# Kernel optimization log

Hardware: AMD Instinct MI355X
Metric: run time of the kernel (lower is better)

The kernel has to match this reference:

```python
import jax, jax.numpy as jnp
import numpy as np

B, S, D = 4, 2048, 1024
H, DK, DV = 16, 64, 64


def setup_inputs() -> dict:
    key = jax.random.key(0)
    ks = jax.random.split(key, 7)
    scale = 0.02
    emb = jax.random.normal(ks[0], (B, S, D), dtype=jnp.float32)
    # per-head projection weights stacked over heads: [H, D, DK/DV]
    Wq = jax.random.normal(ks[1], (H, D, DK), dtype=jnp.float32) * scale
    Wk = jax.random.normal(ks[2], (H, D, DK), dtype=jnp.float32) * scale
    Wv = jax.random.normal(ks[3], (H, D, DV), dtype=jnp.float32) * scale
    # output projection (nn.Linear(d_model, d_model)): weight [D, D] (input-major) + bias
    Wo = jax.random.normal(ks[4], (D, D), dtype=jnp.float32) * scale
    bo = jax.random.normal(ks[5], (D,), dtype=jnp.float32) * scale
    return {"emb": emb, "Wq": Wq, "Wk": Wk, "Wv": Wv, "Wo": Wo, "bo": bo}


def reference(emb, Wq, Wk, Wv, Wo, bo):
    # Per-head projections, batched over heads: [B,H,S,dk]
    q = jnp.einsum("bsd,hdk->bhsk", emb, Wq)
    k = jnp.einsum("bsd,hdk->bhsk", emb, Wk)
    v = jnp.einsum("bsd,hdv->bhsv", emb, Wv)
    # Scaled dot-product with causal mask (bool_mask=True)
    scores = jnp.einsum("bhqk,bhsk->bhqs", q, k) * (DK ** -0.5)  # [B,H,S,S]
    causal = jnp.tril(jnp.ones((S, S), dtype=bool))
    scores = jnp.where(causal, scores, jnp.finfo(scores.dtype).min)
    attn = jax.nn.softmax(scores, axis=-1)
    out = jnp.einsum("bhqs,bhsv->bhqv", attn, v)  # [B,H,S,DV]
    # concat heads -> [B,S,H*DV] == [B,S,D]
    out = out.transpose(0, 2, 1, 3).reshape(B, S, H * DV)
    # output projection; dropout=0.0 -> identity
    return out @ Wo + bo
```

## Files before the change

### kernel.cpp

```cpp
#include <hip/hip_runtime.h>
#include <hip/hip_bf16.h>


typedef __attribute__((ext_vector_type(8))) short bf16x8;
typedef __attribute__((ext_vector_type(4))) float f32x4;
typedef __attribute__((ext_vector_type(4))) unsigned int u32x4;
typedef __attribute__((ext_vector_type(2))) unsigned int u32x2;

#define MFMA16(a, b, c) __builtin_amdgcn_mfma_f32_16x16x32_bf16((a), (b), (c), 0, 0, 0)

#define LOG2E 1.44269504088896340736f
#define BIG_NEG (-3.0e38f)
#define DEFER_THR 10.0f

__device__ __forceinline__ unsigned short f2bf(float f) {
  union { float f; unsigned int i; } x; x.f = f;
  unsigned int lsb = (x.i >> 16) & 1;
  x.i += 0x7fffu + lsb;
  return (unsigned short)(x.i >> 16);
}

__device__ __forceinline__ unsigned int cvtpk(float lo, float hi) {
  unsigned int r;
  asm("v_cvt_pk_bf16_f32 %0, %1, %2" : "=v"(r) : "v"(lo), "v"(hi));
  return r;
}

__device__ __forceinline__ void gl16(const unsigned short* g, void* l) {
  __builtin_amdgcn_global_load_lds(
      (const __attribute__((address_space(1))) unsigned int*)g,
      (__attribute__((address_space(3))) unsigned int*)l, 16, 0, 0);
}

__global__ void wtrans_kernel(const float* __restrict__ in,
                              unsigned short* __restrict__ out, int R, int C) {
  __shared__ unsigned short tile[32][33];
  const int bz = blockIdx.z;
  const int c0 = blockIdx.x * 32, r0 = blockIdx.y * 32;
  const float* ip = in + (size_t)bz * R * C;
  unsigned short* op = out + (size_t)bz * R * C;
  const int tx = threadIdx.x, ty = threadIdx.y;
#pragma unroll
  for (int i = 0; i < 32; i += 8)
    tile[ty + i][tx] = f2bf(ip[(size_t)(r0 + ty + i) * C + (c0 + tx)]);
  __syncthreads();
#pragma unroll
  for (int i = 0; i < 32; i += 8)
    op[(size_t)(c0 + ty + i) * R + (r0 + tx)] = tile[tx][ty + i];
}

__global__ __launch_bounds__(256)
void embconv_kernel(const float* __restrict__ in, unsigned short* __restrict__ out) {
  const int i = blockIdx.x * 256 + threadIdx.x;
  const float4 a = ((const float4*)in)[2 * i];
  const float4 b = ((const float4*)in)[2 * i + 1];
  union { unsigned short u[8]; u32x4 v; } p;
  p.u[0] = f2bf(a.x); p.u[1] = f2bf(a.y); p.u[2] = f2bf(a.z); p.u[3] = f2bf(a.w);
  p.u[4] = f2bf(b.x); p.u[5] = f2bf(b.y); p.u[6] = f2bf(b.z); p.u[7] = f2bf(b.w);
  ((u32x4*)out)[i] = p.v;
}

__global__ __launch_bounds__(256)
void qkv_kernel(const unsigned short* __restrict__ embB,
                const unsigned short* __restrict__ WqT,
                const unsigned short* __restrict__ WkT,
                const unsigned short* __restrict__ WvT,
                unsigned short* __restrict__ QG,
                unsigned short* __restrict__ KG,
                unsigned short* __restrict__ VtG) {
  const int nwg = gridDim.x;
  const int wg = blockIdx.x;
  const int swz = (wg & 7) * (nwg >> 3) + (wg >> 3);
  const int mb = swz / 24;
  const int rem = swz - mb * 24;
  const int t = rem >> 3;
  const int m0 = mb * 128;
  const int n0 = (rem & 7) * 128;
  const int b = m0 >> 11;
  const int sloc = m0 & 2047;
  const unsigned short* Wt =
      (t == 0 ? WqT : (t == 1 ? WkT : WvT)) + (size_t)(n0 >> 6) * 64 * 1024;

  __shared__ __align__(16) unsigned short As[128 * 32];
  __shared__ __align__(16) unsigned short Bs[128 * 32];

  const int tid = threadIdx.x;
  const int lane = tid & 63, w = tid >> 6;
  const int q4 = lane >> 4, l16 = lane & 15;
  const int lr = lane >> 2, lc = (lane & 3) * 8;

  f32x4 acc[4][4] = {};

  const unsigned short* ga0 = &embB[(size_t)(m0 + w * 32 + lr) * 1024 + lc];
  const unsigned short* ga1 = ga0 + 16 * 1024;
  const unsigned short* gb0 = &Wt[(size_t)(w * 32 + lr) * 1024 + lc];
  const unsigned short* gb1 = gb0 + 16 * 1024;
  char* la0 = (char*)As + w * 2048;
  char* lb0 = (char*)Bs + w * 2048;

  for (int k0 = 0; k0 < 1024; k0 += 32) {
    __syncthreads();
    gl16(ga0 + k0, la0);
    gl16(ga1 + k0, la0 + 1024);
    gl16(gb0 + k0, lb0);
    gl16(gb1 + k0, lb0 + 1024);
    __syncthreads();

    const unsigned short* PA = (t == 2) ? Bs : As;
    const unsigned short* PB = (t == 2) ? As : Bs;

    bf16x8 af[4], bfr[4];
#pragma unroll
    for (int ms = 0; ms < 4; ++ms)
      af[ms] = *(const bf16x8*)&PA[((w >> 1) * 64 + ms * 16 + l16) * 32 + q4 * 8];
#pragma unroll
    for (int js = 0; js < 4; ++js)
      bfr[js] = *(const bf16x8*)&PB[((w & 1) * 64 + js * 16 + l16) * 32 + q4 * 8];
    __builtin_amdgcn_s_setprio(1);
#pragma unroll
    for (int ms = 0; ms < 4; ++ms)
#pragma unroll
      for (int js = 0; js < 4; ++js)
        acc[ms][js] = MFMA16(af[ms], bfr[js], acc[ms][js]);
    __builtin_amdgcn_s_setprio(0);
  }

  if (t < 2) {
    unsigned short* outp = (t == 0) ? QG : KG;
    const float osc = (t == 0) ? (0.125f * LOG2E) : 1.0f;
    const int h = (n0 >> 6) + (w & 1);
    const size_t hb = (size_t)(b * 16 + h) * 2048;
#pragma unroll
    for (int ms = 0; ms < 4; ++ms)
#pragma unroll
      for (int js = 0; js < 4; ++js) {
        const int c = js * 16 + l16;
#pragma unroll
        for (int r = 0; r < 4; ++r) {
          const int s = sloc + (w >> 1) * 64 + ms * 16 + q4 * 4 + r;
          outp[(hb + s) * 64 + c] = f2bf(acc[ms][js][r] * osc);
        }
      }
  } else {
    const int h = (n0 >> 6) + (w >> 1);
    const size_t hb = (size_t)(b * 16 + h) * 64;
#pragma unroll
    for (int ms = 0; ms < 4; ++ms)
#pragma unroll
      for (int js = 0; js < 4; ++js) {
        const int s = sloc + (w & 1) * 64 + js * 16 + l16;
#pragma unroll
        for (int r = 0; r < 4; ++r) {
          const int c = ms * 16 + q4 * 4 + r;
          VtG[(hb + c) * 2048 + s] = f2bf(acc[ms][js][r]);
        }
      }
  }
}

__global__ __launch_bounds__(512)
void flash_kernel(const unsigned short* __restrict__ QG,
                  const unsigned short* __restrict__ KG,
                  const unsigned short* __restrict__ VtG,
                  unsigned short* __restrict__ ObG) {
  const int bh = blockIdx.x;
  const int x = blockIdx.y;
  const int q0B = (31 - x) * 64;
  const int tid = threadIdx.x;
  const int lane = tid & 63, w = tid >> 6;
  const int wp = w & 3;
  const int q0w = (w < 4) ? q0B : x * 64;
  const int q4 = lane >> 4, l16 = lane & 15;

  const unsigned short* Qp = QG + ((size_t)bh * 2048 + q0w + wp * 16) * 64;
  const unsigned short* Kp = KG + (size_t)bh * 2048 * 64;
  const unsigned short* Vp = VtG + (size_t)bh * 64 * 2048;

  const bf16x8 qf0 = *(const bf16x8*)&Qp[(size_t)l16 * 64 + q4 * 8];
  const bf16x8 qf1 = *(const bf16x8*)&Qp[(size_t)l16 * 64 + 32 + q4 * 8];

  __shared__ __align__(16) unsigned short Ks[64][72];
  __shared__ __align__(16) unsigned short Vs[64][72];
  __shared__ __align__(16) unsigned short Plds[8][16][72];

  f32x4 oacc[4] = {};
  float m_i = BIG_NEG, l_i = 0.f;

  const int sr = tid >> 3, sc = (tid & 7) * 8;
  u32x4 kreg = *(const u32x4*)&Kp[(size_t)sr * 64 + sc];
  u32x4 vreg = *(const u32x4*)&Vp[(size_t)sr * 2048 + sc];

  for (int j0 = 0; j0 <= q0B; j0 += 64) {
    *(u32x4*)&Ks[sr][sc] = kreg;
    *(u32x4*)&Vs[sr][sc] = vreg;
    __syncthreads();

    if (j0 + 64 <= q0B) {
      const int jn = j0 + 64;
      kreg = *(const u32x4*)&Kp[(size_t)(jn + sr) * 64 + sc];
      vreg = *(const u32x4*)&Vp[(size_t)sr * 2048 + jn + sc];
    }

    if (j0 <= q0w) {
      f32x4 sacc[4] = {};
      __builtin_amdgcn_s_setprio(1);
#pragma unroll
      for (int js = 0; js < 4; ++js) {
        const bf16x8 kf0 = *(const bf16x8*)&Ks[js * 16 + l16][q4 * 8];
        const bf16x8 kf1 = *(const bf16x8*)&Ks[js * 16 + l16][32 + q4 * 8];
        sacc[js] = MFMA16(kf0, qf0, sacc[js]);
        sacc[js] = MFMA16(kf1, qf1, sacc[js]);
      }
      __builtin_amdgcn_s_setprio(0);

      float mloc = BIG_NEG;
      if (j0 == q0w) {
        const int qrel = wp * 16 + l16;
#pragma unroll
        for (int js = 0; js < 4; ++js)
#pragma unroll
          for (int r = 0; r < 4; ++r) {
            const int krel = js * 16 + q4 * 4 + r;
            float v = sacc[js][r];
            if (krel > qrel) v = BIG_NEG;
            sacc[js][r] = v;
            mloc = fmaxf(mloc, v);
          }
      } else {
#pragma unroll
        for (int js = 0; js < 4; ++js)
#pragma unroll
          for (int r = 0; r < 4; ++r) mloc = fmaxf(mloc, sacc[js][r]);
      }
      mloc = fmaxf(mloc, __shfl_xor(mloc, 16, 64));
      mloc = fmaxf(mloc, __shfl_xor(mloc, 32, 64));

      if (__any(mloc > m_i + DEFER_THR)) {
        const float mnew = fmaxf(m_i, mloc);
        const float alpha = __builtin_amdgcn_exp2f(m_i - mnew);
        m_i = mnew;
        l_i *= alpha;
#pragma unroll
        for (int js = 0; js < 4; ++js)
#pragma unroll
          for (int r = 0; r < 4; ++r) oacc[js][r] *= alpha;
      }

      float sm = 0.f;
#pragma unroll
      for (int js = 0; js < 4; ++js)
#pragma unroll
        for (int r = 0; r < 4; ++r) {
          const float p = __builtin_amdgcn_exp2f(sacc[js][r] - m_i);
          sacc[js][r] = p;
          sm += p;
        }
      sm += __shfl_xor(sm, 16, 64);
      sm += __shfl_xor(sm, 32, 64);
      l_i += sm;

#pragma unroll
      for (int js = 0; js < 4; ++js) {
        u32x2 pk;
        pk[0] = cvtpk(sacc[js][0], sacc[js][1]);
        pk[1] = cvtpk(sacc[js][2], sacc[js][3]);
        *(u32x2*)&Plds[w][l16][js * 16 + q4 * 4] = pk;
      }

      asm volatile("" ::: "memory");

      const bf16x8 pf0 = *(const bf16x8*)&Plds[w][l16][q4 * 8];
      const bf16x8 pf1 = *(const bf16x8*)&Plds[w][l16][32 + q4 * 8];

      __builtin_amdgcn_s_setprio(1);
#pragma unroll
      for (int js = 0; js < 4; ++js) {
        const bf16x8 vf0 = *(const bf16x8*)&Vs[js * 16 + l16][q4 * 8];
        const bf16x8 vf1 = *(const bf16x8*)&Vs[js * 16 + l16][32 + q4 * 8];
        oacc[js] = MFMA16(vf0, pf0, oacc[js]);
        oacc[js] = MFMA16(vf1, pf1, oacc[js]);
      }
      __builtin_amdgcn_s_setprio(0);
    }
    __syncthreads();
  }

  const int b = bh >> 4, h = bh & 15;
  const int q = q0w + wp * 16 + l16;
  const float rl = 1.0f / l_i;
  unsigned short* orow = ObG + ((size_t)b * 2048 + q) * 1024 + h * 64;
#pragma unroll
  for (int js = 0; js < 4; ++js) {
    u32x2 ok;
    ok[0] = cvtpk(oacc[js][0] * rl, oacc[js][1] * rl);
    ok[1] = cvtpk(oacc[js][2] * rl, oacc[js][3] * rl);
    *(u32x2*)&orow[js * 16 + q4 * 4] = ok;
  }
}

__global__ __launch_bounds__(256)
void oproj_kernel(const unsigned short* __restrict__ ObG,
                  const unsigned short* __restrict__ WoT,
                  const float* __restrict__ bo,
                  float* __restrict__ outG) {
  const int nwg = gridDim.x;
  const int wg = blockIdx.x;
  const int swz = (wg & 7) * (nwg >> 3) + (wg >> 3);
  const int m0 = (swz >> 3) * 128;
  const int n0 = (swz & 7) * 128;

  __shared__ __align__(16) unsigned short As[128 * 32];
  __shared__ __align__(16) unsigned short Bs[128 * 32];

  const int tid = threadIdx.x;
  const int lane = tid & 63, w = tid >> 6;
  const int q4 = lane >> 4, l16 = lane & 15;
  const int lr = lane >> 2, lc = (lane & 3) * 8;

  f32x4 acc[4][4] = {};

  const unsigned short* ga0 = &ObG[(size_t)(m0 + w * 32 + lr) * 1024 + lc];
  const unsigned short* ga1 = ga0 + 16 * 1024;
  const unsigned short* gb0 = &WoT[(size_t)(n0 + w * 32 + lr) * 1024 + lc];
  const unsigned short* gb1 = gb0 + 16 * 1024;
  char* la0 = (char*)As + w * 2048;
  char* lb0 = (char*)Bs + w * 2048;

  for (int k0 = 0; k0 < 1024; k0 += 32) {
    __syncthreads();
    gl16(ga0 + k0, la0);
    gl16(ga1 + k0, la0 + 1024);
    gl16(gb0 + k0, lb0);
    gl16(gb1 + k0, lb0 + 1024);
    __syncthreads();

    bf16x8 af[4], bfr[4];
#pragma unroll
    for (int ms = 0; ms < 4; ++ms)
      af[ms] = *(const bf16x8*)&As[((w >> 1) * 64 + ms * 16 + l16) * 32 + q4 * 8];
#pragma unroll
    for (int js = 0; js < 4; ++js)
      bfr[js] = *(const bf16x8*)&Bs[((w & 1) * 64 + js * 16 + l16) * 32 + q4 * 8];
    __builtin_amdgcn_s_setprio(1);
#pragma unroll
    for (int ms = 0; ms < 4; ++ms)
#pragma unroll
      for (int js = 0; js < 4; ++js)
        acc[ms][js] = MFMA16(af[ms], bfr[js], acc[ms][js]);
    __builtin_amdgcn_s_setprio(0);
  }

#pragma unroll
  for (int js = 0; js < 4; ++js) {
    const int col = n0 + (w & 1) * 64 + js * 16 + l16;
    const float bias = bo[col];
#pragma unroll
    for (int ms = 0; ms < 4; ++ms)
#pragma unroll
      for (int r = 0; r < 4; ++r) {
        const int row = m0 + (w >> 1) * 64 + ms * 16 + q4 * 4 + r;
        outG[(size_t)row * 1024 + col] = acc[ms][js][r] + bias;
      }
  }
}

extern "C" void kernel_launch(void* const* d_in, const int* in_sizes, int n_in,
                              void* d_out, int out_size, void* d_ws, size_t ws_size,
                              hipStream_t stream) {
  const float* emb = (const float*)d_in[0];
  const float* Wq  = (const float*)d_in[1];
  const float* Wk  = (const float*)d_in[2];
  const float* Wv  = (const float*)d_in[3];
  const float* Wo  = (const float*)d_in[4];
  const float* bo  = (const float*)d_in[5];
  float* out = (float*)d_out;

  char* ws = (char*)d_ws;
  const size_t MB = 1024 * 1024;

  const int nb = (ws_size >= 72 * MB) ? 4 : (ws_size >= 40 * MB) ? 2 : 1;

  unsigned short* WqT = (unsigned short*)(ws + 0 * MB);
  unsigned short* WkT = (unsigned short*)(ws + 2 * MB);
  unsigned short* WvT = (unsigned short*)(ws + 4 * MB);
  unsigned short* WoT = (unsigned short*)(ws + 6 * MB);
  unsigned short* QG  = (unsigned short*)(ws + 8 * MB);
  unsigned short* KG  = (unsigned short*)(ws + (8 + 4 * nb) * MB);
  unsigned short* VtG = (unsigned short*)(ws + (8 + 8 * nb) * MB);
  unsigned short* ObG = (unsigned short*)(ws + (8 + 12 * nb) * MB);

  const dim3 tb(32, 8, 1);
  wtrans_kernel<<<dim3(2, 32, 16), tb, 0, stream>>>(Wq, WqT, 1024, 64);
  wtrans_kernel<<<dim3(2, 32, 16), tb, 0, stream>>>(Wk, WkT, 1024, 64);
  wtrans_kernel<<<dim3(2, 32, 16), tb, 0, stream>>>(Wv, WvT, 1024, 64);
  wtrans_kernel<<<dim3(32, 32, 1), tb, 0, stream>>>(Wo, WoT, 1024, 1024);

  for (int g = 0; g < 4; g += nb) {
    const float* embG = emb + (size_t)g * 2048 * 1024;
    float* outG = out + (size_t)g * 2048 * 1024;
    unsigned short* embB = ObG;
    embconv_kernel<<<dim3(nb * 1024), 256, 0, stream>>>(embG, embB);
    qkv_kernel<<<dim3(24 * 16 * nb), 256, 0, stream>>>(embB, WqT, WkT, WvT, QG, KG, VtG);
    flash_kernel<<<dim3(16 * nb, 16), 512, 0, stream>>>(QG, KG, VtG, ObG);
    oproj_kernel<<<dim3(8 * 16 * nb), 256, 0, stream>>>(ObG, WoT, bo, outG);
  }
}
```

Baseline: 282.5 us.

## Assign contiguous 128-row query tiles per block with swizzled order, defer row-sum reduction

Measured after the change: 280.4 us. About the same (-0.7%).

```diff
diff --git a/kernel.cpp b/kernel.cpp
--- a/kernel.cpp
+++ b/kernel.cpp
@@ -164,15 +164,19 @@
                   const unsigned short* __restrict__ VtG,
                   unsigned short* __restrict__ ObG) {
   const int bh = blockIdx.x;
-  const int x = blockIdx.y;
-  const int q0B = (31 - x) * 64;
+  const int y = blockIdx.y;
+  const int k4 = y >> 2, y0 = y & 3;
+  const int t = k4 + 4 * ((y0 + k4) & 3);
+  const int q0 = t * 128;
   const int tid = threadIdx.x;
   const int lane = tid & 63, w = tid >> 6;
   const int wp = w & 3;
-  const int q0w = (w < 4) ? q0B : x * 64;
   const int q4 = lane >> 4, l16 = lane & 15;
-
-  const unsigned short* Qp = QG + ((size_t)bh * 2048 + q0w + wp * 16) * 64;
+  const int qw = q0 + w * 16;
+  const int jlim = q0 + ((w >= 4) ? 64 : 0);
+  const int jlimB = q0 + 64;
+
+  const unsigned short* Qp = QG + ((size_t)bh * 2048 + qw) * 64;
   const unsigned short* Kp = KG + (size_t)bh * 2048 * 64;
   const unsigned short* Vp = VtG + (size_t)bh * 64 * 2048;
 
@@ -184,24 +188,24 @@
   __shared__ __align__(16) unsigned short Plds[8][16][72];
 
   f32x4 oacc[4] = {};
-  float m_i = BIG_NEG, l_i = 0.f;
+  float m_i = BIG_NEG, l_part = 0.f;
 
   const int sr = tid >> 3, sc = (tid & 7) * 8;
   u32x4 kreg = *(const u32x4*)&Kp[(size_t)sr * 64 + sc];
   u32x4 vreg = *(const u32x4*)&Vp[(size_t)sr * 2048 + sc];
 
-  for (int j0 = 0; j0 <= q0B; j0 += 64) {
+  for (int j0 = 0; j0 <= jlimB; j0 += 64) {
     *(u32x4*)&Ks[sr][sc] = kreg;
     *(u32x4*)&Vs[sr][sc] = vreg;
     __syncthreads();
 
-    if (j0 + 64 <= q0B) {
+    if (j0 + 64 <= jlimB) {
       const int jn = j0 + 64;
       kreg = *(const u32x4*)&Kp[(size_t)(jn + sr) * 64 + sc];
       vreg = *(const u32x4*)&Vp[(size_t)sr * 2048 + jn + sc];
     }
 
-    if (j0 <= q0w) {
+    if (j0 <= jlim) {
       f32x4 sacc[4] = {};
       __builtin_amdgcn_s_setprio(1);
 #pragma unroll
@@ -214,7 +218,7 @@
       __builtin_amdgcn_s_setprio(0);
 
       float mloc = BIG_NEG;
-      if (j0 == q0w) {
+      if (j0 == jlim) {
         const int qrel = wp * 16 + l16;
 #pragma unroll
         for (int js = 0; js < 4; ++js)
@@ -239,25 +243,21 @@
         const float mnew = fmaxf(m_i, mloc);
         const float alpha = __builtin_amdgcn_exp2f(m_i - mnew);
         m_i = mnew;
-        l_i *= alpha;
+        l_part *= alpha;
 #pragma unroll
         for (int js = 0; js < 4; ++js)
 #pragma unroll
           for (int r = 0; r < 4; ++r) oacc[js][r] *= alpha;
       }
 
-      float sm = 0.f;
 #pragma unroll
       for (int js = 0; js < 4; ++js)
 #pragma unroll
         for (int r = 0; r < 4; ++r) {
           const float p = __builtin_amdgcn_exp2f(sacc[js][r] - m_i);
           sacc[js][r] = p;
-          sm += p;
+          l_part += p;
         }
-      sm += __shfl_xor(sm, 16, 64);
-      sm += __shfl_xor(sm, 32, 64);
-      l_i += sm;
 
 #pragma unroll
       for (int js = 0; js < 4; ++js) {
@@ -285,8 +285,12 @@
     __syncthreads();
   }
 
+  float l_i = l_part;
+  l_i += __shfl_xor(l_i, 16, 64);
+  l_i += __shfl_xor(l_i, 32, 64);
+
   const int b = bh >> 4, h = bh & 15;
-  const int q = q0w + wp * 16 + l16;
+  const int q = qw + l16;
   const float rl = 1.0f / l_i;
   unsigned short* orow = ObG + ((size_t)b * 2048 + q) * 1024 + h * 64;
 #pragma unroll
```
